# Optimization experiments

Hardware: AMD Instinct MI355X
Metric: run time of the kernel (lower is better)

The kernel has to match this reference:

```python
import jax, jax.numpy as jnp
import numpy as np
import math

WIN = 7
N = WIN * WIN            # 49 tokens per window
DIM = 192
HEADS = 6
HEAD_DIM = DIM // HEADS  # 32
B_ = 4096                # batch * num_windows
NUM_WIN = 64             # windows per image (mask leading dim)
TABLE = (2 * WIN - 1) ** 2  # 169


def _rel_pos_index(wh, ww):
    coords = np.stack(np.meshgrid(np.arange(wh), np.arange(ww), indexing='ij'))  # [2,wh,ww]
    cf = coords.reshape(2, -1)                       # [2, N]
    rc = (cf[:, :, None] - cf[:, None, :]).transpose(1, 2, 0).astype(np.int32)  # [N,N,2]
    rc[:, :, 0] += wh - 1
    rc[:, :, 1] += ww - 1
    rc[:, :, 0] *= 2 * ww - 1
    return rc.sum(-1)                                # [N,N] in [0, TABLE)


def setup_inputs() -> dict:
    key = jax.random.key(0)
    ks = jax.random.split(key, 6)
    x = jax.random.normal(ks[0], (B_, N, DIM), dtype=jnp.float32)
    # shifted-window style 0/-100 mask
    m = jax.random.uniform(ks[1], (NUM_WIN, N, N))
    mask = jnp.where(m < 0.8, 0.0, -100.0).astype(jnp.float32)
    qkv_w = jax.random.normal(ks[2], (3 * DIM, DIM), dtype=jnp.float32) * 0.02
    qkv_b = jnp.zeros((3 * DIM,), dtype=jnp.float32)
    logit_scale = jnp.full((HEADS, 1, 1), math.log(10.0), dtype=jnp.float32)
    rel_bias_table = jax.random.normal(ks[3], (TABLE, HEADS), dtype=jnp.float32) * 0.02
    rel_index = jnp.asarray(_rel_pos_index(WIN, WIN), dtype=jnp.int32)
    proj_w = jax.random.normal(ks[4], (DIM, DIM), dtype=jnp.float32) * 0.02
    proj_b = jnp.zeros((DIM,), dtype=jnp.float32)
    return {"x": x, "mask": mask, "qkv_w": qkv_w, "qkv_b": qkv_b,
            "logit_scale": logit_scale, "rel_bias_table": rel_bias_table,
            "rel_index": rel_index, "proj_w": proj_w, "proj_b": proj_b}


def reference(x, mask, qkv_w, qkv_b, logit_scale, rel_bias_table, rel_index, proj_w, proj_b):
    B, n, C = x.shape
    H = logit_scale.shape[0]
    qkv = (jnp.einsum('bnc,oc->bno', x, qkv_w) + qkv_b).reshape(B, n, 3, H, -1)
    qkv = jnp.transpose(qkv, (2, 0, 3, 1, 4))  # [3,B,H,n,hd]
    q, k, v = qkv[0], qkv[1], qkv[2]
    # cosine attention: l2-normalize q and k (torch F.normalize, eps=1e-12)
    qn = q / jnp.maximum(jnp.linalg.norm(q, axis=-1, keepdims=True), 1e-12)
    kn = k / jnp.maximum(jnp.linalg.norm(k, axis=-1, keepdims=True), 1e-12)
    attn = jnp.einsum('bhnd,bhmd->bhnm', qn, kn)
    scale = jnp.exp(jnp.minimum(logit_scale, math.log(1.0 / 0.01)))  # [H,1,1]
    attn = attn * scale
    # gathered relative position bias -> [1,H,n,n]
    bias = rel_bias_table[rel_index.reshape(-1)].reshape(n, n, H)
    attn = attn + jnp.transpose(bias, (2, 0, 1))[None]
    nw = mask.shape[0]
    attn = attn.reshape(B // nw, nw, H, n, n) + mask[None, :, None]
    attn = jax.nn.softmax(attn.reshape(B, H, n, n), axis=-1)
    out = jnp.einsum('bhnm,bhmd->bhnd', attn, v)
    out = jnp.transpose(out, (0, 2, 1, 3)).reshape(B, n, -1)
    return jnp.einsum('bnc,oc->bno', out, proj_w) + proj_b
```

## Files before the change

kernel.cpp:

```cpp
#include <hip/hip_runtime.h>
#include <hip/hip_fp16.h>


#define NTOK 49
#define DIM 192
#define NH 6
#define BATCH 4096
#define MTOT 200704

typedef __attribute__((ext_vector_type(4))) float f32x4;
typedef __attribute__((ext_vector_type(8))) _Float16 f16x8;
typedef __attribute__((ext_vector_type(4))) _Float16 f16x4h;

#define W1_OFF 0
#define W2_OFF 221184
#define BMI_OFF 294912
#define HSC_OFF 2260992
#define Q_OFF 4194304
#define K_OFF 81264640
#define V_OFF 158334976

#define LOG2E 1.44269504088896f

#define MFMA16(a, b, c) __builtin_amdgcn_mfma_f32_16x16x32_f16(a, b, c, 0, 0, 0)

#define GLOAD_LDS16(gsrc, ldst)                                      \
  __builtin_amdgcn_global_load_lds(                                  \
      (const __attribute__((address_space(1))) unsigned int*)(gsrc), \
      (__attribute__((address_space(3))) unsigned int*)(ldst), 16, 0, 0)

__global__ __launch_bounds__(256) void k_setup(
    const float* __restrict__ qkv_w, const float* __restrict__ proj_w,
    const float* __restrict__ mask, const float* __restrict__ table,
    const int* __restrict__ rel_index, const float* __restrict__ ls,
    char* __restrict__ W1s, _Float16* __restrict__ W2,
    _Float16* __restrict__ bmi, float* __restrict__ hsc) {
  int idx = blockIdx.x * 256 + threadIdx.x;
  if (idx < 576 * 192) {
    int col = idx / 192, kk = idx - col * 192;
    unsigned int o = (unsigned int)(col & 31) * 384 + (unsigned int)kk * 2;
    unsigned int d = (unsigned int)(col >> 5) * 12288 +
                     (o ^ (((unsigned int)col & 7) << 4));
    *(_Float16*)(W1s + d) = (_Float16)qkv_w[idx];
  }
  if (idx < 192 * 192) W2[idx] = (_Float16)proj_w[idx];
  if (idx < NH) hsc[idx] = __expf(fminf(ls[idx], 4.60517019f)) * LOG2E;
  if (idx < 64 * NH * 2401) {
    int p = idx / 2401, rem = idx % 2401;
    int i = rem / 49, j = rem % 49;
    int wdx = p / NH, h = p % NH;
    bmi[(size_t)p * 2548 + i * 52 + j] =
        (_Float16)((table[rel_index[i * 49 + j] * NH + h] +
                    mask[wdx * 2401 + i * 49 + j]) * LOG2E);
  }
}

__global__ __launch_bounds__(256, 2) void k_qkv(
    const float* __restrict__ x, const char* __restrict__ W1s,
    const float* __restrict__ qkv_b, _Float16* __restrict__ q16,
    _Float16* __restrict__ k16, _Float16* __restrict__ v16) {
  __shared__ __align__(16) char wlds[2][36864];

  const int tid = threadIdx.x;
  const int lane = tid & 63;
  const int w = tid >> 6;
  const int rowbase = blockIdx.x * 256 + w * 64;
  const int L = lane & 15;
  const int g = lane >> 4;

  f16x8 ax[4][6];
#pragma unroll
  for (int rt = 0; rt < 4; ++rt) {
    const float* xr = x + (size_t)(rowbase + rt * 16 + L) * DIM + 8 * g;
#pragma unroll
    for (int kf = 0; kf < 6; ++kf) {
      f32x4 lo = *(const f32x4*)(xr + 32 * kf);
      f32x4 hi = *(const f32x4*)(xr + 32 * kf + 4);
      f16x8 v;
      v[0] = (_Float16)lo[0]; v[1] = (_Float16)lo[1];
      v[2] = (_Float16)lo[2]; v[3] = (_Float16)lo[3];
      v[4] = (_Float16)hi[0]; v[5] = (_Float16)hi[1];
      v[6] = (_Float16)hi[2]; v[7] = (_Float16)hi[3];
      ax[rt][kf] = v;
    }
  }
  int qkb[4][4];
#pragma unroll
  for (int rt = 0; rt < 4; ++rt)
#pragma unroll
    for (int r = 0; r < 4; ++r) {
      int row = rowbase + rt * 16 + 4 * g + r;
      int bb = row / 49, n = row - bb * 49;
      qkb[rt][r] = bb * 9408 + n * 32;
    }

#pragma unroll
  for (int r = 0; r < 9; ++r)
    GLOAD_LDS16(W1s + (w * 9 + r) * 1024 + lane * 16,
                &wlds[0][(w * 9 + r) * 1024]);

#pragma unroll 1
  for (int grp = 0; grp < 6; ++grp) {
    __syncthreads();
    const int cur = grp & 1;

    if (grp < 5) {
#pragma unroll
      for (int r = 0; r < 9; ++r)
        GLOAD_LDS16(W1s + (size_t)(grp + 1) * 36864 + (w * 9 + r) * 1024 +
                        lane * 16,
                    &wlds[cur ^ 1][(w * 9 + r) * 1024]);
    }

    const unsigned int sw = (unsigned int)(L & 7) << 4;
#pragma unroll
    for (int tl = 0; tl < 3; ++tl) {
      const int t = grp * 3 + tl;
      const int s = t / 6;
      const int tt = t - 6 * s;
      _Float16* dst = (s == 0) ? q16 : (s == 1) ? k16 : v16;
      const char* base = &wlds[cur][tl * 12288];
#pragma unroll
      for (int ct = 0; ct < 2; ++ct) {
        f16x8 wf[6];
#pragma unroll
        for (int kf = 0; kf < 6; ++kf) {
          unsigned int o0 = (unsigned int)(16 * ct + L) * 384 +
                            (unsigned int)kf * 64 + (unsigned int)g * 16;
          wf[kf] = *(const f16x8*)(base + (o0 ^ sw));
        }
        f32x4 acc[4];
#pragma unroll
        for (int rt = 0; rt < 4; ++rt) acc[rt] = (f32x4){0.f, 0.f, 0.f, 0.f};
#pragma unroll
        for (int kf = 0; kf < 6; ++kf)
#pragma unroll
          for (int rt = 0; rt < 4; ++rt)
            acc[rt] = MFMA16(ax[rt][kf], wf[kf], acc[rt]);
        const float bias = qkv_b[192 * s + 32 * tt + 16 * ct + L];
        const int off = tt * 1568 + 16 * ct + L;
#pragma unroll
        for (int rt = 0; rt < 4; ++rt)
#pragma unroll
          for (int r = 0; r < 4; ++r)
            dst[qkb[rt][r] + off] = (_Float16)(acc[rt][r] + bias);
      }
    }
  }
}

__global__ __launch_bounds__(768, 6) void k_attn2(
    const _Float16* __restrict__ q16, const _Float16* __restrict__ k16,
    const _Float16* __restrict__ v16, const _Float16* __restrict__ bmi,
    const float* __restrict__ hsc, const _Float16* __restrict__ W2,
    const float* __restrict__ proj_b, float* __restrict__ out) {
  __shared__ __align__(16) _Float16 pl[12][16 * 80];
  __shared__ __align__(16) _Float16 ao[2][64 * 200];

  const int tid = threadIdx.x;
  const int wv = tid >> 6;
  const int ww = wv / 6;
  const int h = wv - 6 * ww;
  const int b = blockIdx.x * 2 + ww;
  const int lane = tid & 63;
  const int L = lane & 15;
  const int g = lane >> 4;

  const size_t qoff = ((size_t)b * NH + h) * 1568;
  const float hs = hsc[h];

  f16x8 vf[2][2];
#pragma unroll
  for (int dt = 0; dt < 2; ++dt)
#pragma unroll
    for (int kf = 0; kf < 2; ++kf)
#pragma unroll
      for (int e = 0; e < 8; ++e) {
        int j = 32 * kf + 8 * g + e;
        if (j > 48) j = 48;
        vf[dt][kf][e] = v16[qoff + j * 32 + 16 * dt + L];
      }

  f16x8 kf4[4];
#pragma unroll
  for (int jt = 0; jt < 4; ++jt) {
    int jrow = 16 * jt + L; if (jrow > 48) jrow = 48;
    kf4[jt] = *(const f16x8*)(k16 + qoff + jrow * 32 + 8 * g);
    float kk = 0.f;
#pragma unroll
    for (int e = 0; e < 8; ++e) kk += (float)kf4[jt][e] * (float)kf4[jt][e];
    kk += __shfl_xor(kk, 16);
    kk += __shfl_xor(kk, 32);
    const float inv = rsqrtf(fmaxf(kk, 1e-24f));
#pragma unroll
    for (int e = 0; e < 8; ++e)
      kf4[jt][e] = (_Float16)((float)kf4[jt][e] * inv);
  }

  _Float16* plw = &pl[wv][0];
  const _Float16* bmp = bmi + ((size_t)(b & 63) * NH + h) * 2548;

#pragma unroll 1
  for (int it = 0; it < 4; ++it) {
    int irow = 16 * it + L; if (irow > 48) irow = 48;
    f16x8 qf = *(const f16x8*)(q16 + qoff + irow * 32 + 8 * g);
    float qq = 0.f;
#pragma unroll
    for (int e = 0; e < 8; ++e) qq += (float)qf[e] * (float)qf[e];
    qq += __shfl_xor(qq, 16);
    qq += __shfl_xor(qq, 32);
    const float qr = rsqrtf(fmaxf(qq, 1e-24f)) * hs;

    f32x4 st[4];
#pragma unroll
    for (int jt = 0; jt < 4; ++jt) {
      f32x4 z = {0.f, 0.f, 0.f, 0.f};
      st[jt] = MFMA16(kf4[jt], qf, z);
    }
    const _Float16* bp = bmp + (16 * it + L) * 52 + 4 * g;
#pragma unroll
    for (int jt = 0; jt < 4; ++jt) {
      f16x4h bm4 = *(const f16x4h*)(bp + 16 * jt);
#pragma unroll
      for (int r = 0; r < 4; ++r) {
        int j = 16 * jt + 4 * g + r;
        st[jt][r] = (j < NTOK) ? fmaf(st[jt][r], qr, (float)bm4[r]) : -1e30f;
      }
    }
    float mx = st[0][0];
#pragma unroll
    for (int jt = 0; jt < 4; ++jt)
#pragma unroll
      for (int r = 0; r < 4; ++r) mx = fmaxf(mx, st[jt][r]);
    mx = fmaxf(mx, __shfl_xor(mx, 16));
    mx = fmaxf(mx, __shfl_xor(mx, 32));
    float sum = 0.f;
#pragma unroll
    for (int jt = 0; jt < 4; ++jt)
#pragma unroll
      for (int r = 0; r < 4; ++r) {
        st[jt][r] = exp2f(st[jt][r] - mx);
        sum += st[jt][r];
      }
    sum += __shfl_xor(sum, 16);
    sum += __shfl_xor(sum, 32);
    const float is = 1.0f / sum;

#pragma unroll
    for (int jt = 0; jt < 4; ++jt) {
      f16x4h pk;
#pragma unroll
      for (int r = 0; r < 4; ++r) pk[r] = (_Float16)(st[jt][r] * is);
      *(f16x4h*)(plw + L * 80 + 16 * jt + 4 * g) = pk;
    }
    f16x8 pa0 = *(const f16x8*)(plw + L * 80 + 8 * g);
    f16x8 pa1 = *(const f16x8*)(plw + L * 80 + 32 + 8 * g);
#pragma unroll
    for (int dt = 0; dt < 2; ++dt) {
      f32x4 o4 = {0.f, 0.f, 0.f, 0.f};
      o4 = MFMA16(pa0, vf[dt][0], o4);
      o4 = MFMA16(pa1, vf[dt][1], o4);
#pragma unroll
      for (int r = 0; r < 4; ++r)
        ao[ww][(16 * it + 4 * g + r) * 200 + 32 * h + 16 * dt + L] =
            (_Float16)o4[r];
    }
  }
  __syncthreads();

#pragma unroll
  for (int cp = 0; cp < 2; ++cp) {
    const int ct = h + 6 * cp;
    const _Float16* wp = W2 + (size_t)(16 * ct + L) * DIM + 8 * g;
    f16x8 wfr[6];
#pragma unroll
    for (int kf = 0; kf < 6; ++kf) wfr[kf] = *(const f16x8*)(wp + 32 * kf);
    const float pbv = proj_b[16 * ct + L];
#pragma unroll 1
    for (int mt = 0; mt < 4; ++mt) {
      f32x4 acc = {0.f, 0.f, 0.f, 0.f};
#pragma unroll
      for (int kf = 0; kf < 6; ++kf) {
        f16x8 af =
            *(const f16x8*)(&ao[ww][(16 * mt + L) * 200 + 32 * kf + 8 * g]);
        acc = MFMA16(af, wfr[kf], acc);
      }
#pragma unroll
      for (int r = 0; r < 4; ++r) {
        int row = 16 * mt + 4 * g + r;
        if (row < NTOK)
          out[((size_t)b * NTOK + row) * DIM + 16 * ct + L] = acc[r] + pbv;
      }
    }
  }
}

extern "C" void kernel_launch(void* const* d_in, const int* in_sizes, int n_in,
                              void* d_out, int out_size, void* d_ws, size_t ws_size,
                              hipStream_t stream) {
  const float* x     = (const float*)d_in[0];
  const float* mask  = (const float*)d_in[1];
  const float* qkv_w = (const float*)d_in[2];
  const float* qkv_b = (const float*)d_in[3];
  const float* ls    = (const float*)d_in[4];
  const float* tbl   = (const float*)d_in[5];
  const int*   ridx  = (const int*)d_in[6];
  const float* pw    = (const float*)d_in[7];
  const float* pb    = (const float*)d_in[8];
  float* out = (float*)d_out;
  char* ws = (char*)d_ws;

  char* W1s = ws + W1_OFF;
  _Float16* W2 = (_Float16*)(ws + W2_OFF);
  _Float16* bmi = (_Float16*)(ws + BMI_OFF);
  float* hsc = (float*)(ws + HSC_OFF);
  _Float16* q16 = (_Float16*)(ws + Q_OFF);
  _Float16* k16 = (_Float16*)(ws + K_OFF);
  _Float16* v16 = (_Float16*)(ws + V_OFF);

  hipLaunchKernelGGL(k_setup, dim3(3602), dim3(256), 0, stream,
                     qkv_w, pw, mask, tbl, ridx, ls, W1s, W2, bmi, hsc);
  hipLaunchKernelGGL(k_qkv, dim3(MTOT / 256), dim3(256), 0, stream,
                     x, W1s, qkv_b, q16, k16, v16);
  hipLaunchKernelGGL(k_attn2, dim3(BATCH / 2), dim3(768), 0, stream,
                     q16, k16, v16, bmi, hsc, W2, pb, out);
}
```

Baseline: 255.0 us.

## Store V transposed with padded rows and swizzle the P tile in LDS

The QKV kernel now writes V transposed per head (head-dim rows padded to 56 tokens), so the attention kernel loads V fragments as single 16-byte vectors instead of 16 scalar gathers per fragment. The per-wave P staging buffer also gets a 128-byte row pitch with an XOR swizzle, meant to cut LDS bank conflicts on the P store and reload. In exchange, the V stores in the QKV kernel become strided and less coalesced. The padding slots for tokens 49..55 are never written, so those lanes read uninitialized workspace, which is only safe if P is exactly zero there and the garbage is not NaN.

```diff
diff --git a/kernel.cpp b/kernel.cpp
--- a/kernel.cpp
+++ b/kernel.cpp
@@ -18,7 +18,7 @@
 #define HSC_OFF 2260992
 #define Q_OFF 4194304
 #define K_OFF 81264640
-#define V_OFF 158334976
+#define VT_OFF 158334976
 
 #define LOG2E 1.44269504088896f
 
@@ -58,7 +58,7 @@
 __global__ __launch_bounds__(256, 2) void k_qkv(
     const float* __restrict__ x, const char* __restrict__ W1s,
     const float* __restrict__ qkv_b, _Float16* __restrict__ q16,
-    _Float16* __restrict__ k16, _Float16* __restrict__ v16) {
+    _Float16* __restrict__ k16, _Float16* __restrict__ vt16) {
   __shared__ __align__(16) char wlds[2][36864];
 
   const int tid = threadIdx.x;
@@ -84,7 +84,7 @@
       ax[rt][kf] = v;
     }
   }
-  int qkb[4][4];
+  int qkb[4][4], vts[4][4];
 #pragma unroll
   for (int rt = 0; rt < 4; ++rt)
 #pragma unroll
@@ -92,6 +92,7 @@
       int row = rowbase + rt * 16 + 4 * g + r;
       int bb = row / 49, n = row - bb * 49;
       qkb[rt][r] = bb * 9408 + n * 32;
+      vts[rt][r] = bb * 10752 + n;
     }
 
 #pragma unroll
@@ -118,7 +119,6 @@
       const int t = grp * 3 + tl;
       const int s = t / 6;
       const int tt = t - 6 * s;
-      _Float16* dst = (s == 0) ? q16 : (s == 1) ? k16 : v16;
       const char* base = &wlds[cur][tl * 12288];
 #pragma unroll
       for (int ct = 0; ct < 2; ++ct) {
@@ -138,12 +138,22 @@
           for (int rt = 0; rt < 4; ++rt)
             acc[rt] = MFMA16(ax[rt][kf], wf[kf], acc[rt]);
         const float bias = qkv_b[192 * s + 32 * tt + 16 * ct + L];
-        const int off = tt * 1568 + 16 * ct + L;
-#pragma unroll
-        for (int rt = 0; rt < 4; ++rt)
-#pragma unroll
-          for (int r = 0; r < 4; ++r)
-            dst[qkb[rt][r] + off] = (_Float16)(acc[rt][r] + bias);
+        if (s < 2) {
+          _Float16* dst = (s == 0) ? q16 : k16;
+          const int off = tt * 1568 + 16 * ct + L;
+#pragma unroll
+          for (int rt = 0; rt < 4; ++rt)
+#pragma unroll
+            for (int r = 0; r < 4; ++r)
+              dst[qkb[rt][r] + off] = (_Float16)(acc[rt][r] + bias);
+        } else {
+          const int off = tt * 1792 + (16 * ct + L) * 56;
+#pragma unroll
+          for (int rt = 0; rt < 4; ++rt)
+#pragma unroll
+            for (int r = 0; r < 4; ++r)
+              vt16[vts[rt][r] + off] = (_Float16)(acc[rt][r] + bias);
+        }
       }
     }
   }
@@ -151,10 +161,10 @@
 
 __global__ __launch_bounds__(768, 6) void k_attn2(
     const _Float16* __restrict__ q16, const _Float16* __restrict__ k16,
-    const _Float16* __restrict__ v16, const _Float16* __restrict__ bmi,
+    const _Float16* __restrict__ vt16, const _Float16* __restrict__ bmi,
     const float* __restrict__ hsc, const _Float16* __restrict__ W2,
     const float* __restrict__ proj_b, float* __restrict__ out) {
-  __shared__ __align__(16) _Float16 pl[12][16 * 80];
+  __shared__ __align__(128) _Float16 pl[12][1024];
   __shared__ __align__(16) _Float16 ao[2][64 * 200];
 
   const int tid = threadIdx.x;
@@ -167,6 +177,7 @@
   const int g = lane >> 4;
 
   const size_t qoff = ((size_t)b * NH + h) * 1568;
+  const size_t voff = ((size_t)b * NH + h) * 1792;
   const float hs = hsc[h];
 
   f16x8 vf[2][2];
@@ -174,12 +185,8 @@
   for (int dt = 0; dt < 2; ++dt)
 #pragma unroll
     for (int kf = 0; kf < 2; ++kf)
-#pragma unroll
-      for (int e = 0; e < 8; ++e) {
-        int j = 32 * kf + 8 * g + e;
-        if (j > 48) j = 48;
-        vf[dt][kf][e] = v16[qoff + j * 32 + 16 * dt + L];
-      }
+      vf[dt][kf] =
+          *(const f16x8*)(vt16 + voff + (16 * dt + L) * 56 + 32 * kf + 8 * g);
 
   f16x8 kf4[4];
 #pragma unroll
@@ -197,7 +204,9 @@
       kf4[jt][e] = (_Float16)((float)kf4[jt][e] * inv);
   }
 
-  _Float16* plw = &pl[wv][0];
+  char* plw = (char*)&pl[wv][0];
+  const unsigned int pswz =
+      (((unsigned int)L & 1) << 6) | (((unsigned int)L & 12) << 2);
   const _Float16* bmp = bmi + ((size_t)(b & 63) * NH + h) * 2548;
 
 #pragma unroll 1
@@ -251,10 +260,13 @@
       f16x4h pk;
 #pragma unroll
       for (int r = 0; r < 4; ++r) pk[r] = (_Float16)(st[jt][r] * is);
-      *(f16x4h*)(plw + L * 80 + 16 * jt + 4 * g) = pk;
-    }
-    f16x8 pa0 = *(const f16x8*)(plw + L * 80 + 8 * g);
-    f16x8 pa1 = *(const f16x8*)(plw + L * 80 + 32 + 8 * g);
+      *(f16x4h*)(plw +
+                 (((unsigned int)L * 128 + 32u * jt + 8u * g) ^ pswz)) = pk;
+    }
+    f16x8 pa0 =
+        *(const f16x8*)(plw + (((unsigned int)L * 128 + 16u * g) ^ pswz));
+    f16x8 pa1 = *(const f16x8*)(plw +
+                                (((unsigned int)L * 128 + 64 + 16u * g) ^ pswz));
 #pragma unroll
     for (int dt = 0; dt < 2; ++dt) {
       f32x4 o4 = {0.f, 0.f, 0.f, 0.f};
@@ -316,12 +328,12 @@
   float* hsc = (float*)(ws + HSC_OFF);
   _Float16* q16 = (_Float16*)(ws + Q_OFF);
   _Float16* k16 = (_Float16*)(ws + K_OFF);
-  _Float16* v16 = (_Float16*)(ws + V_OFF);
+  _Float16* vt16 = (_Float16*)(ws + VT_OFF);
 
   hipLaunchKernelGGL(k_setup, dim3(3602), dim3(256), 0, stream,
                      qkv_w, pw, mask, tbl, ridx, ls, W1s, W2, bmi, hsc);
   hipLaunchKernelGGL(k_qkv, dim3(MTOT / 256), dim3(256), 0, stream,
-                     x, W1s, qkv_b, q16, k16, v16);
+                     x, W1s, qkv_b, q16, k16, vt16);
   hipLaunchKernelGGL(k_attn2, dim3(BATCH / 2), dim3(768), 0, stream,
-                     q16, k16, v16, bmi, hsc, W2, pb, out);
+                     q16, k16, vt16, bmi, hsc, W2, pb, out);
 }
```

Measured after the change: 383.0 us. 1.5x slower.
